# Kernel optimization log

Hardware: AMD Instinct MI355X
Metric: run time of the kernel (lower is better)

The kernel has to match this reference:

```python
import jax, jax.numpy as jnp
import numpy as np

T, B, D, NH, DH, MEM = 1024, 4, 1024, 8, 128, 1024
LIM = 1024  # PositionalEmbedding lim default


def setup_inputs() -> dict:
    key = jax.random.key(0)
    ks = jax.random.split(key, 11)
    h = jax.random.normal(ks[0], (T, B, D), jnp.float32)
    m = jax.random.normal(ks[1], (MEM, B, D), jnp.float32)
    q_w = jax.random.normal(ks[2], (NH * DH, D), jnp.float32) * 0.02
    k_w = jax.random.normal(ks[3], (NH * DH, D), jnp.float32) * 0.02
    r_w = jax.random.normal(ks[4], (NH * DH, D), jnp.float32) * 0.02
    k_bias = jax.random.normal(ks[5], (NH, DH), jnp.float32)  # torch init normal(0,1)
    r_bias = jax.random.normal(ks[6], (NH, DH), jnp.float32)
    ln_scale = jnp.ones((D,), jnp.float32)
    ln_bias = jnp.zeros((D,), jnp.float32)
    reset = jax.random.uniform(ks[7], (T, B)) < 0.01       # sparse episode resets
    old_reset = jax.random.uniform(ks[8], (MEM, B)) < 0.01
    return dict(h=h, m=m, q_w=q_w, k_w=k_w, r_w=r_w, k_bias=k_bias, r_bias=r_bias,
                ln_scale=ln_scale, ln_bias=ln_bias, reset=reset, old_reset=old_reset)


def layer_norm(x, scale, bias, eps=1e-5):
    mu = jnp.mean(x, axis=-1, keepdims=True)
    var = jnp.mean(jnp.square(x - mu), axis=-1, keepdims=True)
    return (x - mu) * jax.lax.rsqrt(var + eps) * scale + bias


def rel_shift(x):
    # x: [T, C, B, N] -> Transformer-XL relative shift
    t, c = x.shape[:2]
    tail = x.shape[2:]
    zero_pad = jnp.zeros((t, 1) + tail, x.dtype)
    x_padded = jnp.concatenate([zero_pad, x], axis=1).reshape((c + 1, t) + tail)
    return x_padded[1:].reshape(x.shape)


def reference(h, m, q_w, k_w, r_w, k_bias, r_bias, ln_scale, ln_bias, reset, old_reset):
    t, b = h.shape[:2]
    mm = m.shape[0]
    tm = t + mm
    # ---- ResetMasker: cols[i,b,j] = any reset at i' with j < i' <= i ----
    resets = jnp.concatenate([old_reset, reset], 0).astype(jnp.int32)  # [L, B]
    cum = jnp.cumsum(resets, axis=0)                                   # [L, B]
    reset_mask = (cum[-t:, None, :] - cum[None, :, :]) > 0             # [T, L, B]
    reset_mask = reset_mask[:, -tm:]                                   # [T, TM, B]
    # ---- default attention mask ----
    i = jnp.arange(t)[:, None]
    j = jnp.arange(tm)[None, :]
    mask_len = mm + t - MEM
    mask_shift_len = (t - mask_len) if mask_len > 0 else t
    future_mask = j >= i + mm          # triu(ones, M + future=0)
    history_mask = j <= i - mask_shift_len
    default_mask = (future_mask | history_mask)[:, :, None]            # [T, TM, 1]
    mask = (reset_mask | default_mask)[:, :, :, None]                  # [T, TM, B, 1]
    # ---- projections ----
    cat = layer_norm(jnp.concatenate([m, h], axis=0), ln_scale, ln_bias)  # [TM, B, D]
    q = (cat[-t:] @ q_w.T).reshape(t, b, NH, DH)
    k = (cat @ k_w.T).reshape(tm, b, NH, DH)
    score = jnp.einsum('ibnd,jbnd->ijbn', q + k_bias, k)               # [T, TM, B, NH]
    # ---- relative position term ----
    pos_seq = jnp.arange(tm - 1, -1, -1, dtype=h.dtype)
    inv_freq = 2.0 * jnp.pi / LIM ** (jnp.arange(0, D, 2, dtype=jnp.float32) / D)
    sinusoid = pos_seq[:, None] * inv_freq                              # [TM, D/2]
    pe = jnp.concatenate([jnp.sin(sinusoid), jnp.cos(sinusoid)], -1)    # [TM, D]
    r = (pe @ r_w.T).reshape(tm, NH, DH)
    pos_score = jnp.einsum('ibnd,jnd->ijbn', q + r_bias, r)             # [T, TM, B, NH]
    score = score + rel_shift(pos_score)
    # ---- scale, mask, clamp, softmax ----
    score = jnp.where(mask, -65000.0, score / np.sqrt(DH))
    score = jnp.clip(score, -65000.0, 65000.0)
    prob = jax.nn.softmax(score, axis=1)
    all_masked = jnp.all(mask, axis=1, keepdims=True)                   # [T, 1, B, 1]
    return jnp.where(all_masked, 0.0, prob)
```

## Files before the change

### kernel.cpp

```cpp
#include <hip/hip_runtime.h>
#include <hip/hip_bf16.h>
#include <stdint.h>

typedef __bf16 bf16;
typedef __bf16 bf16x4 __attribute__((ext_vector_type(4)));
typedef __bf16 bf16x8 __attribute__((ext_vector_type(8)));
typedef float f32x4 __attribute__((ext_vector_type(4)));

__device__ __forceinline__ void gload_lds16(const void* g, void* l) {
  __builtin_amdgcn_global_load_lds((const __attribute__((address_space(1))) void*)g,
                                   (__attribute__((address_space(3))) void*)l, 16, 0, 0);
}

__global__ void setup_kernel(const void* __restrict__ rst, const void* __restrict__ orst,
                             int* __restrict__ jmin) {
  __shared__ int sflag;
  int tid = threadIdx.x;
  if (tid == 0) sflag = 0;
  __syncthreads();
  int local = 0;
  for (int idx = tid; idx < 1024; idx += 256) {
    unsigned v1 = ((const unsigned*)rst)[idx];
    unsigned v2 = ((const unsigned*)orst)[idx];
    unsigned vv[2] = {v1, v2};
    for (int t = 0; t < 2; ++t) {
      unsigned v = vv[t];
      if (v == 0x3F800000u) local |= 1;
      else if (v > 1u) local |= 2;
    }
  }
  if (local) atomicOr(&sflag, local);
  __syncthreads();
  int mode = (sflag & 2) ? 2 : ((sflag & 1) ? 1 : 0);
  int lane = tid & 63, w = tid >> 6;
  if (w < 4) {
    int b = w;
    int rv[32];
    int lmax = -1;
#pragma unroll
    for (int u = 0; u < 32; ++u) {
      int s = lane * 32 + u;
      int idx = (s < 1024) ? s * 4 + b : (s - 1024) * 4 + b;
      const void* p = (s < 1024) ? orst : rst;
      int x;
      if (mode == 2)      x = ((const unsigned char*)p)[idx] != 0;
      else if (mode == 1) x = ((const float*)p)[idx] != 0.0f;
      else                x = ((const int*)p)[idx] != 0;
      rv[u] = x;
      if (x) lmax = s;
    }
    int inc = lmax;
    for (int o = 1; o < 64; o <<= 1) {
      int oth = __shfl_up(inc, o);
      if (lane >= o && oth > inc) inc = oth;
    }
    int cur = __shfl_up(inc, 1);
    if (lane == 0) cur = -1;
#pragma unroll
    for (int u = 0; u < 32; ++u) {
      int s = lane * 32 + u;
      if (rv[u]) cur = s;
      if (s >= 1024) jmin[(s - 1024) * 4 + b] = (cur > 0) ? cur : 0;
    }
  }
}

__global__ __launch_bounds__(256) void ln_kernel(const float* __restrict__ h, const float* __restrict__ mm,
                                                 const float* __restrict__ sc, const float* __restrict__ bi,
                                                 bf16* __restrict__ catln) {
  int row = blockIdx.x;
  const float* src = (row < 4096) ? (mm + (size_t)row * 1024) : (h + (size_t)(row - 4096) * 1024);
  int tid = threadIdx.x;
  float4 v = ((const float4*)src)[tid];
  float s1 = v.x + v.y + v.z + v.w;
  float s2 = v.x * v.x + v.y * v.y + v.z * v.z + v.w * v.w;
  int lane = tid & 63, w = tid >> 6;
  for (int o = 32; o; o >>= 1) { s1 += __shfl_down(s1, o); s2 += __shfl_down(s2, o); }
  __shared__ float red[8];
  if (lane == 0) { red[w] = s1; red[w + 4] = s2; }
  __syncthreads();
  float S1 = red[0] + red[1] + red[2] + red[3];
  float S2 = red[4] + red[5] + red[6] + red[7];
  float mean = S1 * (1.0f / 1024.0f);
  float var = S2 * (1.0f / 1024.0f) - mean * mean;
  float rstd = rsqrtf(var + 1e-5f);
  bf16x4 o;
#pragma unroll
  for (int c = 0; c < 4; ++c) {
    float x = (c == 0) ? v.x : (c == 1) ? v.y : (c == 2) ? v.z : v.w;
    o[c] = (bf16)((x - mean) * rstd * sc[tid * 4 + c] + bi[tid * 4 + c]);
  }
  *(bf16x4*)(catln + (size_t)row * 1024 + tid * 4) = o;
}

__global__ __launch_bounds__(256) void prep_kernel(const float* __restrict__ qw, const float* __restrict__ kw,
                                                   const float* __restrict__ rw, bf16* __restrict__ qwb,
                                                   bf16* __restrict__ kwb, bf16* __restrict__ rwb,
                                                   bf16* __restrict__ pe) {
  size_t id = (size_t)blockIdx.x * 256 + threadIdx.x;
  if (id < 3145728) {
    const float* s = id < 1048576 ? qw : (id < 2097152 ? kw : rw);
    bf16* d = id < 1048576 ? qwb : (id < 2097152 ? kwb : rwb);
    size_t o = id & 1048575;
    d[o] = (bf16)s[o];
  } else {
    size_t p = id - 3145728;
    int jj = (int)(p >> 10), dcol = (int)(p & 1023);
    float pos = (float)(2047 - jj);
    int fi = dcol < 512 ? dcol : dcol - 512;
    float f = exp2f(-0.01953125f * (float)fi);
    float rev = pos * f;
    rev -= floorf(rev);
    float ang = 6.283185307179586f * rev;
    pe[p] = (bf16)(dcol < 512 ? __sinf(ang) : __cosf(ang));
  }
}

__device__ __forceinline__ size_t out_index(int mode, int row, int col) {
  int n = col >> 7, dh = col & 127;
  if (mode <= 0) { int i = row >> 2, b = row & 3; return ((size_t)(b * 8 + n) * 1024 + i) * 128 + dh; }
  if (mode == 1) { int s = row >> 2, b = row & 3; return ((size_t)(b * 8 + n) * 2048 + s) * 128 + dh; }
  return ((size_t)n * 2048 + row) * 128 + dh;
}

__global__ __launch_bounds__(256) void gemm_all(const bf16* __restrict__ catln, const bf16* __restrict__ pe,
                                                const bf16* __restrict__ qwb, const bf16* __restrict__ kwb,
                                                const bf16* __restrict__ rwb, const float* __restrict__ kbias,
                                                const float* __restrict__ rbias, bf16* __restrict__ qkb,
                                                bf16* __restrict__ qrb, bf16* __restrict__ kkv,
                                                bf16* __restrict__ rrv) {
  __shared__ alignas(16) char lA[8192];
  __shared__ alignas(16) char lB[8192];
  const int K = 1024;
  int by = blockIdx.y;
  const bf16* A; const bf16* W; int mode; int brow;
  if (by < 32)      { mode = 0; A = catln + (size_t)4096 * 1024; W = qwb; brow = by << 7; }
  else if (by < 96) { mode = 1; A = catln;                        W = kwb; brow = (by - 32) << 7; }
  else              { mode = 2; A = pe;                           W = rwb; brow = (by - 96) << 7; }
  int tid = threadIdx.x;
  int lane = tid & 63, w = tid >> 6;
  int bcol = blockIdx.x << 7;
  int wr = w >> 1, wc = w & 1;
  f32x4 acc[4][4] = {};
  int r0 = tid >> 2;
  int c8 = (tid & 3) << 3;
  const bf16* gA0 = A + (size_t)(brow + r0) * K + c8;
  const bf16* gB0 = W + (size_t)(bcol + r0) * K + c8;
  char* lAw = lA + w * 1024;
  char* lBw = lB + w * 1024;
  for (int k0 = 0; k0 < K; k0 += 32) {
    if (k0) __syncthreads();
    gload_lds16(gA0 + k0, lAw);
    gload_lds16(gA0 + (size_t)64 * K + k0, lAw + 4096);
    gload_lds16(gB0 + k0, lBw);
    gload_lds16(gB0 + (size_t)64 * K + k0, lBw + 4096);
    __syncthreads();
    const char* pa = lA + (((wr << 6) + (lane & 15)) << 6) + ((lane >> 4) << 4);
    const char* pb = lB + (((wc << 6) + (lane & 15)) << 6) + ((lane >> 4) << 4);
    bf16x8 af[4], bfr[4];
#pragma unroll
    for (int x = 0; x < 4; ++x) {
      af[x] = *(const bf16x8*)(pa + (x << 10));
      bfr[x] = *(const bf16x8*)(pb + (x << 10));
    }
#pragma unroll
    for (int mi = 0; mi < 4; ++mi)
#pragma unroll
      for (int ni = 0; ni < 4; ++ni)
        acc[mi][ni] = __builtin_amdgcn_mfma_f32_16x16x32_bf16(af[mi], bfr[ni], acc[mi][ni], 0, 0, 0);
  }
  int rowb = brow + (wr << 6) + ((lane >> 4) << 2);
  int colb = bcol + (wc << 6) + (lane & 15);
#pragma unroll
  for (int mi = 0; mi < 4; ++mi)
#pragma unroll
    for (int ni = 0; ni < 4; ++ni) {
      int col = colb + (ni << 4);
      float bk = 0.0f, br = 0.0f;
      if (mode == 0) { bk = kbias[col]; br = rbias[col]; }
#pragma unroll
      for (int v = 0; v < 4; ++v) {
        int row = rowb + (mi << 4) + v;
        size_t idx = out_index(mode, row, col);
        if (mode == 0) {
          qkb[idx] = (bf16)(acc[mi][ni][v] + bk);
          qrb[idx] = (bf16)(acc[mi][ni][v] + br);
        } else if (mode == 1) {
          kkv[idx] = (bf16)acc[mi][ni][v];
        } else {
          rrv[idx] = (bf16)acc[mi][ni][v];
        }
      }
    }
}

__global__ __launch_bounds__(256, 2) void score2_kernel(const bf16* __restrict__ qk, const bf16* __restrict__ qr,
                                                        const bf16* __restrict__ kk, const bf16* __restrict__ rr,
                                                        const int* __restrict__ jmin, bf16* __restrict__ P,
                                                        float* __restrict__ scaleBuf) {
  __shared__ float sl[64 * 128];
  __shared__ alignas(16) bf16 stg[2][64 * 128];
  __shared__ int jl_s[64];
  int tid = threadIdx.x, lane = tid & 63;
  int w = (tid >> 6) & 3;
  int bid0 = blockIdx.x;
  int bid = ((bid0 & 7) << 7) | (bid0 >> 3);
  int bn = bid >> 5;
  int it = (bid >> 1) & 15;
  int hh = bid & 1;
  int i0 = it << 6;
  int b = bn >> 3, n = bn & 7;
  int r15 = lane & 15, kc = lane >> 4;
  int il0 = w << 4;
  int g4 = kc << 2;
  const float scale = 0.08838834764831845f;

  if (tid < 64) jl_s[tid] = jmin[(i0 + tid) * 4 + b];

  bf16x8 aK[4], aR[4];
  {
    const bf16* qkrow = qk + ((size_t)bn * 1024 + i0 + il0 + r15) * 128 + kc * 8;
    const bf16* qrrow = qr + ((size_t)bn * 1024 + i0 + il0 + r15) * 128 + kc * 8;
#pragma unroll
    for (int ks = 0; ks < 4; ++ks) {
      aK[ks] = *(const bf16x8*)(qkrow + ks * 32);
      aR[ks] = *(const bf16x8*)(qrrow + ks * 32);
    }
  }

  int su1 = tid, su2 = tid + 256;
  int srow1 = su1 >> 4, scol1 = (su1 & 15) ^ (srow1 & 7);
  int srow2 = su2 >> 4, scol2 = (su2 & 15) ^ (srow2 & 7);
  size_t do1 = (size_t)(su1 & ~63) * 16;
  size_t do2 = (size_t)(su2 & ~63) * 16;
  const bf16* rbase = rr + (size_t)n * 2048 * 128;
  const bf16* kbase = kk + (size_t)bn * 2048 * 128;

  auto issue_pair = [&](int pg) {
    if (pg >= 20) return;
    char* bufb = (char*)stg + (size_t)(pg & 1) * 16384;
#pragma unroll
    for (int k = 0; k < 2; ++k) {
      int ti = pg * 2 + k;
      int ci = ti / 10, si = ti - ci * 10;
      int gc = (hh << 2) + ci;
      const bf16* base = (si < 4) ? rbase : kbase;
      int row0 = (si < 4) ? (1023 + (gc << 7) + (si << 5)) : (i0 + (gc << 7) + ((si - 4) << 5));
      char* db = bufb + (size_t)k * 8192;
      gload_lds16(base + (size_t)(row0 + srow1) * 128 + scol1 * 8, db + do1);
      gload_lds16(base + (size_t)(row0 + srow2) * 128 + scol2 * 8, db + do2);
    }
  };

  int xsw = (((il0 >> 2) + kc) & 7) << 4;
  f32x4 s2r[8];

  issue_pair(0);
  for (int cl = 0; cl < 4; ++cl) {
    int gc = (hh << 2) + cl;
    int c128 = gc << 7;
#pragma unroll
    for (int q = 0; q < 5; ++q) {
      int g = cl * 5 + q;
      __syncthreads();
      issue_pair(g + 1);
      const char* pb = (const char*)stg + (size_t)(g & 1) * 16384;
      __builtin_amdgcn_s_setprio(1);
      if (q < 2) {
#pragma unroll
        for (int sc = 0; sc < 4; ++sc) {
          const char* sb = pb + (sc >> 1) * 8192;
          int fr = ((sc & 1) << 4) + r15;
          f32x4 acc = {};
#pragma unroll
          for (int ks = 0; ks < 4; ++ks) {
            int lcol = (ks << 2) + kc;
            bf16x8 bf = *(const bf16x8*)(sb + fr * 256 + ((lcol ^ (fr & 7)) << 4));
            acc = __builtin_amdgcn_mfma_f32_16x16x32_bf16(aR[ks], bf, acc, 0, 0, 0);
          }
          s2r[q * 4 + sc] = acc;
        }
      } else {
#pragma unroll
        for (int sc = 0; sc < 4; ++sc) {
          int jl0 = ((q - 2) << 6) + (sc << 4);
          int doff = jl0 - il0;
          if (doff < -15 || doff > 142) continue;
          const char* sb = pb + (sc >> 1) * 8192;
          int fr = ((sc & 1) << 4) + r15;
          f32x4 acc = {};
#pragma unroll
          for (int ks = 0; ks < 4; ++ks) {
            int lcol = (ks << 2) + kc;
            bf16x8 bf = *(const bf16x8*)(sb + fr * 256 + ((lcol ^ (fr & 7)) << 4));
            acc = __builtin_amdgcn_mfma_f32_16x16x32_bf16(aK[ks], bf, acc, 0, 0, 0);
          }
          int dbase = jl0 + r15 - il0 - g4;
#pragma unroll
          for (int v = 0; v < 4; ++v) {
            int ddl = dbase - v;
            if ((unsigned)ddl < 128u) {
              sl[(il0 + g4 + v) * 128 + (ddl ^ xsw)] = acc[v];
            }
          }
        }
      }
      __builtin_amdgcn_s_setprio(0);
      if (q == 4) {
#pragma unroll
        for (int v = 0; v < 4; ++v) {
          int il = il0 + g4 + v;
          int ig = i0 + il;
          int jm = jl_s[il];
          int lo = (ig + 1 > jm) ? ig + 1 : jm;
          int ddlo = lo - ig;
          float vals[8];
          float mx = -3.0e38f;
#pragma unroll
          for (int u = 0; u < 8; ++u) {
            int ddc = (u << 4) + r15;
            float x = (s2r[u][v] + sl[il * 128 + (ddc ^ xsw)]) * scale;
            x = fminf(fmaxf(x, -65000.0f), 65000.0f);
            float xm = ((c128 + ddc) >= ddlo) ? x : -3.0e38f;
            vals[u] = xm;
            mx = fmaxf(mx, xm);
          }
          for (int o = 8; o; o >>= 1) mx = fmaxf(mx, __shfl_xor(mx, o));
          float sum = 0.0f;
#pragma unroll
          for (int u = 0; u < 8; ++u) {
            float e = (vals[u] > -1.0e38f) ? __expf(vals[u] - mx) : 0.0f;
            vals[u] = e;
            sum += e;
          }
          for (int o = 8; o; o >>= 1) sum += __shfl_xor(sum, o);
          size_t pbase = ((size_t)bn * 1024 + ig) * 1024;
#pragma unroll
          for (int u = 0; u < 8; ++u) {
            int dd = c128 + (u << 4) + r15;
            P[pbase + (((dd >> 3) ^ (bn & 7)) << 3) + (dd & 7)] = (bf16)vals[u];
          }
          if (r15 == 0) {
            float2 ms = make_float2(mx, sum);
            *(float2*)(scaleBuf + (((size_t)ig * 32 + bn) * 8 + gc) * 2) = ms;
          }
        }
      }
    }
  }
}

__global__ __launch_bounds__(256) void score_full(const bf16* __restrict__ qk, const bf16* __restrict__ qr,
                                                  const bf16* __restrict__ kk, const bf16* __restrict__ rr,
                                                  const int* __restrict__ jmin, float* __restrict__ out) {
  __shared__ float sl[16 * 1024];
  int tid = threadIdx.x, lane = tid & 63, w = tid >> 6;
  int bid = blockIdx.x;
  int i0 = (bid & 63) << 4;
  int bn = bid >> 6;
  int b = bn >> 3, n = bn & 7;
  int r15 = lane & 15, kc = lane >> 4;
  bf16x8 aq[4], ar[4];
  {
    const bf16* qkrow = qk + ((size_t)bn * 1024 + i0 + r15) * 128 + kc * 8;
    const bf16* qrrow = qr + ((size_t)bn * 1024 + i0 + r15) * 128 + kc * 8;
#pragma unroll
    for (int f = 0; f < 4; ++f) {
      aq[f] = *(const bf16x8*)(qkrow + f * 32);
      ar[f] = *(const bf16x8*)(qrrow + f * 32);
    }
  }
  for (int t = w; t < 64; t += 4) {
    int dd0 = t << 4;
    const bf16* rrow = rr + ((size_t)n * 2048 + 1023 + dd0 + r15) * 128 + kc * 8;
    f32x4 acc = {};
#pragma unroll
    for (int f = 0; f < 4; ++f)
      acc = __builtin_amdgcn_mfma_f32_16x16x32_bf16(ar[f], *(const bf16x8*)(rrow + f * 32), acc, 0, 0, 0);
    int dd = dd0 + r15;
#pragma unroll
    for (int v = 0; v < 4; ++v) sl[(kc * 4 + v) * 1024 + dd] = acc[v];
  }
  __syncthreads();
  for (int t = w; t < 65; t += 4) {
    int j0 = i0 + (t << 4);
    const bf16* krow = kk + ((size_t)bn * 2048 + j0 + r15) * 128 + kc * 8;
    f32x4 acc = {};
#pragma unroll
    for (int f = 0; f < 4; ++f)
      acc = __builtin_amdgcn_mfma_f32_16x16x32_bf16(aq[f], *(const bf16x8*)(krow + f * 32), acc, 0, 0, 0);
    int jc = (t << 4) + r15;
#pragma unroll
    for (int v = 0; v < 4; ++v) {
      int ii = kc * 4 + v;
      int dd = jc - ii;
      if (dd >= 1 && dd <= 1023) sl[ii * 1024 + dd] += acc[v];
    }
  }
  __syncthreads();
  const float scale = 0.08838834764831845f;
  for (int ii = w; ii < 16; ii += 4) {
    int i = i0 + ii;
    int jm = jmin[i * 4 + b];
    int lo = (i + 1 > jm) ? i + 1 : jm;
    int ddlo = lo - i;
    size_t ob = (size_t)i * 65536 + bn;
    if (ddlo > 1023) {
      for (int j = lane; j < 2048; j += 64) out[ob + (size_t)j * 32] = 0.0f;
      continue;
    }
    float vals[16];
    float mx = -3.0e38f;
#pragma unroll
    for (int c = 0; c < 16; ++c) {
      int dd = (c << 6) + lane;
      float x = sl[ii * 1024 + dd] * scale;
      x = fminf(fmaxf(x, -65000.0f), 65000.0f);
      float xm = (dd >= ddlo) ? x : -3.0e38f;
      vals[c] = xm;
      mx = fmaxf(mx, xm);
    }
    for (int o = 32; o; o >>= 1) mx = fmaxf(mx, __shfl_xor(mx, o));
    float sum = 0.0f;
#pragma unroll
    for (int c = 0; c < 16; ++c) {
      float e = (vals[c] > -1.0e38f) ? __expf(vals[c] - mx) : 0.0f;
      vals[c] = e;
      sum += e;
    }
    for (int o = 32; o; o >>= 1) sum += __shfl_xor(sum, o);
    float inv = 1.0f / sum;
    for (int j = lane; j < 2048; j += 64) {
      int dd = j - i;
      float pv = 0.0f;
      if (dd >= ddlo && dd <= 1023) {
        float x = sl[ii * 1024 + dd] * scale;
        x = fminf(fmaxf(x, -65000.0f), 65000.0f);
        pv = __expf(x - mx) * inv;
      }
      out[ob + (size_t)j * 32] = pv;
    }
  }
}

__global__ __launch_bounds__(256) void scatter_kernel(const bf16* __restrict__ P,
                                                      const float* __restrict__ scaleBuf,
                                                      float* __restrict__ out) {
  __shared__ alignas(16) bf16 ld[32 * 1024];
  __shared__ float sc_l[32 * 8];
  int i = blockIdx.x;
  int tid = threadIdx.x;
#pragma unroll
  for (int it = 0; it < 16; ++it) {
    int c = it * 256 + tid;
    int bn = c >> 7, u = c & 127;
    const bf16* src = P + ((size_t)bn * 1024 + i) * 1024 + u * 8;
    gload_lds16(src, (char*)ld + (size_t)(it * 256 + (tid & ~63)) * 16);
  }
  {
    int bn_t = tid >> 3, c_t = tid & 7;
    const float2* sp = (const float2*)(scaleBuf + ((size_t)i * 32 + bn_t) * 16);
    float m[8], s[8];
#pragma unroll
    for (int k = 0; k < 8; ++k) { float2 p = sp[k]; m[k] = p.x; s[k] = p.y; }
    float M = m[0];
#pragma unroll
    for (int k = 1; k < 8; ++k) M = fmaxf(M, m[k]);
    float S = 0.0f;
#pragma unroll
    for (int k = 0; k < 8; ++k) S += s[k] * __expf(m[k] - M);
    sc_l[bn_t * 8 + c_t] = (S > 0.0f) ? (__expf(m[c_t] - M) / S) : 0.0f;
  }
  __syncthreads();
  int bn0 = (tid & 7) << 2;
  int jb = tid >> 3;
  size_t ob = (size_t)i * 65536;
  for (int it = 0; it < 64; ++it) {
    int j = it * 32 + jb;
    int dd = j - i;
    f32x4 v = {0.0f, 0.0f, 0.0f, 0.0f};
    if (dd >= 1 && dd <= 1023) {
      int u = dd >> 3, lo = (dd & 7) << 1, cc = dd >> 7;
#pragma unroll
      for (int e = 0; e < 4; ++e) {
        int bn = bn0 + e;
        const bf16* p = (const bf16*)((const char*)ld + bn * 2048 + (((u ^ (bn & 7)) << 4) | lo));
        v[e] = (float)*p * sc_l[bn * 8 + cc];
      }
    }
    *(f32x4*)(out + ob + (size_t)j * 32 + bn0) = v;
  }
}

extern "C" void kernel_launch(void* const* d_in, const int* in_sizes, int n_in,
                              void* d_out, int out_size, void* d_ws, size_t ws_size,
                              hipStream_t stream) {
  const float* h   = (const float*)d_in[0];
  const float* m   = (const float*)d_in[1];
  const float* qw  = (const float*)d_in[2];
  const float* kw  = (const float*)d_in[3];
  const float* rw  = (const float*)d_in[4];
  const float* kb  = (const float*)d_in[5];
  const float* rb  = (const float*)d_in[6];
  const float* lns = (const float*)d_in[7];
  const float* lnb = (const float*)d_in[8];
  const void*  rst = d_in[9];
  const void* orst = d_in[10];
  float* out = (float*)d_out;
  char* ws = (char*)d_ws;

  int* jmin   = (int*)ws;
  bf16* catln = (bf16*)(ws + 65536);
  bf16* qwb   = catln + (size_t)8192 * 1024;
  bf16* kwb   = qwb + (size_t)1024 * 1024;
  bf16* rwb   = kwb + (size_t)1024 * 1024;
  bf16* pe    = rwb + (size_t)1024 * 1024;
  bf16* qkb   = pe + (size_t)2048 * 1024;
  bf16* qrb   = qkb + (size_t)4096 * 1024;
  bf16* kk    = qrb + (size_t)4096 * 1024;
  bf16* rr    = kk + (size_t)8192 * 1024;
  bf16* P     = rr + (size_t)2048 * 1024;
  float* scaleBuf = (float*)(P + (size_t)33554432);
  size_t need_fast = (size_t)((char*)(scaleBuf + 524288) - ws);
  bool fast = ws_size >= need_fast;

  setup_kernel<<<1, 256, 0, stream>>>(rst, orst, jmin);
  ln_kernel<<<8192, 256, 0, stream>>>(h, m, lns, lnb, catln);
  prep_kernel<<<20480, 256, 0, stream>>>(qw, kw, rw, qwb, kwb, rwb, pe);
  gemm_all<<<dim3(8, 112), 256, 0, stream>>>(catln, pe, qwb, kwb, rwb, kb, rb, qkb, qrb, kk, rr);
  if (fast) {
    score2_kernel<<<1024, 256, 0, stream>>>(qkb, qrb, kk, rr, jmin, P, scaleBuf);
    scatter_kernel<<<1024, 256, 0, stream>>>(P, scaleBuf, out);
  } else {
    score_full<<<2048, 256, 0, stream>>>(qkb, qrb, kk, rr, jmin, out);
  }
}
```

Measured before the change: 218.4 us.

## Fuse preprocessing kernels and vectorize scatter with new LDS swizzle

```diff
diff --git a/kernel.cpp b/kernel.cpp
--- a/kernel.cpp
+++ b/kernel.cpp
@@ -12,107 +12,106 @@
                                    (__attribute__((address_space(3))) void*)l, 16, 0, 0);
 }
 
-__global__ void setup_kernel(const void* __restrict__ rst, const void* __restrict__ orst,
-                             int* __restrict__ jmin) {
-  __shared__ int sflag;
+__global__ __launch_bounds__(256) void pre_kernel(const float* __restrict__ h, const float* __restrict__ mm,
+                                                  const float* __restrict__ sc, const float* __restrict__ bi,
+                                                  bf16* __restrict__ catln, const float* __restrict__ qw,
+                                                  const float* __restrict__ kw, const float* __restrict__ rw,
+                                                  bf16* __restrict__ qwb, bf16* __restrict__ kwb,
+                                                  bf16* __restrict__ rwb, bf16* __restrict__ pe,
+                                                  const void* __restrict__ rst, const void* __restrict__ orst,
+                                                  int* __restrict__ jmin) {
+  int bx = blockIdx.x;
   int tid = threadIdx.x;
-  if (tid == 0) sflag = 0;
-  __syncthreads();
-  int local = 0;
-  for (int idx = tid; idx < 1024; idx += 256) {
-    unsigned v1 = ((const unsigned*)rst)[idx];
-    unsigned v2 = ((const unsigned*)orst)[idx];
-    unsigned vv[2] = {v1, v2};
-    for (int t = 0; t < 2; ++t) {
-      unsigned v = vv[t];
-      if (v == 0x3F800000u) local |= 1;
-      else if (v > 1u) local |= 2;
-    }
-  }
-  if (local) atomicOr(&sflag, local);
-  __syncthreads();
-  int mode = (sflag & 2) ? 2 : ((sflag & 1) ? 1 : 0);
-  int lane = tid & 63, w = tid >> 6;
-  if (w < 4) {
-    int b = w;
-    int rv[32];
-    int lmax = -1;
-#pragma unroll
-    for (int u = 0; u < 32; ++u) {
-      int s = lane * 32 + u;
-      int idx = (s < 1024) ? s * 4 + b : (s - 1024) * 4 + b;
-      const void* p = (s < 1024) ? orst : rst;
-      int x;
-      if (mode == 2)      x = ((const unsigned char*)p)[idx] != 0;
-      else if (mode == 1) x = ((const float*)p)[idx] != 0.0f;
-      else                x = ((const int*)p)[idx] != 0;
-      rv[u] = x;
-      if (x) lmax = s;
-    }
-    int inc = lmax;
-    for (int o = 1; o < 64; o <<= 1) {
-      int oth = __shfl_up(inc, o);
-      if (lane >= o && oth > inc) inc = oth;
-    }
-    int cur = __shfl_up(inc, 1);
-    if (lane == 0) cur = -1;
-#pragma unroll
-    for (int u = 0; u < 32; ++u) {
-      int s = lane * 32 + u;
-      if (rv[u]) cur = s;
-      if (s >= 1024) jmin[(s - 1024) * 4 + b] = (cur > 0) ? cur : 0;
-    }
-  }
-}
-
-__global__ __launch_bounds__(256) void ln_kernel(const float* __restrict__ h, const float* __restrict__ mm,
-                                                 const float* __restrict__ sc, const float* __restrict__ bi,
-                                                 bf16* __restrict__ catln) {
-  int row = blockIdx.x;
-  const float* src = (row < 4096) ? (mm + (size_t)row * 1024) : (h + (size_t)(row - 4096) * 1024);
-  int tid = threadIdx.x;
-  float4 v = ((const float4*)src)[tid];
-  float s1 = v.x + v.y + v.z + v.w;
-  float s2 = v.x * v.x + v.y * v.y + v.z * v.z + v.w * v.w;
-  int lane = tid & 63, w = tid >> 6;
-  for (int o = 32; o; o >>= 1) { s1 += __shfl_down(s1, o); s2 += __shfl_down(s2, o); }
-  __shared__ float red[8];
-  if (lane == 0) { red[w] = s1; red[w + 4] = s2; }
-  __syncthreads();
-  float S1 = red[0] + red[1] + red[2] + red[3];
-  float S2 = red[4] + red[5] + red[6] + red[7];
-  float mean = S1 * (1.0f / 1024.0f);
-  float var = S2 * (1.0f / 1024.0f) - mean * mean;
-  float rstd = rsqrtf(var + 1e-5f);
-  bf16x4 o;
-#pragma unroll
-  for (int c = 0; c < 4; ++c) {
-    float x = (c == 0) ? v.x : (c == 1) ? v.y : (c == 2) ? v.z : v.w;
-    o[c] = (bf16)((x - mean) * rstd * sc[tid * 4 + c] + bi[tid * 4 + c]);
-  }
-  *(bf16x4*)(catln + (size_t)row * 1024 + tid * 4) = o;
-}
-
-__global__ __launch_bounds__(256) void prep_kernel(const float* __restrict__ qw, const float* __restrict__ kw,
-                                                   const float* __restrict__ rw, bf16* __restrict__ qwb,
-                                                   bf16* __restrict__ kwb, bf16* __restrict__ rwb,
-                                                   bf16* __restrict__ pe) {
-  size_t id = (size_t)blockIdx.x * 256 + threadIdx.x;
-  if (id < 3145728) {
-    const float* s = id < 1048576 ? qw : (id < 2097152 ? kw : rw);
-    bf16* d = id < 1048576 ? qwb : (id < 2097152 ? kwb : rwb);
-    size_t o = id & 1048575;
-    d[o] = (bf16)s[o];
+  if (bx < 8192) {
+    int row = bx;
+    const float* src = (row < 4096) ? (mm + (size_t)row * 1024) : (h + (size_t)(row - 4096) * 1024);
+    float4 v = ((const float4*)src)[tid];
+    float s1 = v.x + v.y + v.z + v.w;
+    float s2 = v.x * v.x + v.y * v.y + v.z * v.z + v.w * v.w;
+    int lane = tid & 63, w = tid >> 6;
+    for (int o = 32; o; o >>= 1) { s1 += __shfl_down(s1, o); s2 += __shfl_down(s2, o); }
+    __shared__ float red[8];
+    if (lane == 0) { red[w] = s1; red[w + 4] = s2; }
+    __syncthreads();
+    float S1 = red[0] + red[1] + red[2] + red[3];
+    float S2 = red[4] + red[5] + red[6] + red[7];
+    float mean = S1 * (1.0f / 1024.0f);
+    float var = S2 * (1.0f / 1024.0f) - mean * mean;
+    float rstd = rsqrtf(var + 1e-5f);
+    bf16x4 o;
+#pragma unroll
+    for (int c = 0; c < 4; ++c) {
+      float x = (c == 0) ? v.x : (c == 1) ? v.y : (c == 2) ? v.z : v.w;
+      o[c] = (bf16)((x - mean) * rstd * sc[tid * 4 + c] + bi[tid * 4 + c]);
+    }
+    *(bf16x4*)(catln + (size_t)row * 1024 + tid * 4) = o;
+  } else if (bx < 28672) {
+    size_t id = (size_t)(bx - 8192) * 256 + tid;
+    if (id < 3145728) {
+      const float* s = id < 1048576 ? qw : (id < 2097152 ? kw : rw);
+      bf16* d = id < 1048576 ? qwb : (id < 2097152 ? kwb : rwb);
+      size_t o = id & 1048575;
+      d[o] = (bf16)s[o];
+    } else {
+      size_t p = id - 3145728;
+      int jj = (int)(p >> 10), dcol = (int)(p & 1023);
+      float pos = (float)(2047 - jj);
+      int fi = dcol < 512 ? dcol : dcol - 512;
+      float f = exp2f(-0.01953125f * (float)fi);
+      float rev = pos * f;
+      rev -= floorf(rev);
+      float ang = 6.283185307179586f * rev;
+      pe[p] = (bf16)(dcol < 512 ? __sinf(ang) : __cosf(ang));
+    }
   } else {
-    size_t p = id - 3145728;
-    int jj = (int)(p >> 10), dcol = (int)(p & 1023);
-    float pos = (float)(2047 - jj);
-    int fi = dcol < 512 ? dcol : dcol - 512;
-    float f = exp2f(-0.01953125f * (float)fi);
-    float rev = pos * f;
-    rev -= floorf(rev);
-    float ang = 6.283185307179586f * rev;
-    pe[p] = (bf16)(dcol < 512 ? __sinf(ang) : __cosf(ang));
+    __shared__ int sflag;
+    if (tid == 0) sflag = 0;
+    __syncthreads();
+    int local = 0;
+    for (int idx = tid; idx < 1024; idx += 256) {
+      unsigned v1 = ((const unsigned*)rst)[idx];
+      unsigned v2 = ((const unsigned*)orst)[idx];
+      unsigned vv[2] = {v1, v2};
+      for (int t = 0; t < 2; ++t) {
+        unsigned v = vv[t];
+        if (v == 0x3F800000u) local |= 1;
+        else if (v > 1u) local |= 2;
+      }
+    }
+    if (local) atomicOr(&sflag, local);
+    __syncthreads();
+    int mode = (sflag & 2) ? 2 : ((sflag & 1) ? 1 : 0);
+    int lane = tid & 63, w = tid >> 6;
+    if (w < 4) {
+      int b = w;
+      int rv[32];
+      int lmax = -1;
+#pragma unroll
+      for (int u = 0; u < 32; ++u) {
+        int s = lane * 32 + u;
+        int idx = (s < 1024) ? s * 4 + b : (s - 1024) * 4 + b;
+        const void* p = (s < 1024) ? orst : rst;
+        int x;
+        if (mode == 2)      x = ((const unsigned char*)p)[idx] != 0;
+        else if (mode == 1) x = ((const float*)p)[idx] != 0.0f;
+        else                x = ((const int*)p)[idx] != 0;
+        rv[u] = x;
+        if (x) lmax = s;
+      }
+      int inc = lmax;
+      for (int o = 1; o < 64; o <<= 1) {
+        int oth = __shfl_up(inc, o);
+        if (lane >= o && oth > inc) inc = oth;
+      }
+      int cur = __shfl_up(inc, 1);
+      if (lane == 0) cur = -1;
+#pragma unroll
+      for (int u = 0; u < 32; ++u) {
+        int s = lane * 32 + u;
+        if (rv[u]) cur = s;
+        if (s >= 1024) jmin[(s - 1024) * 4 + b] = (cur > 0) ? cur : 0;
+      }
+    }
   }
 }
 
@@ -214,6 +213,7 @@
   int il0 = w << 4;
   int g4 = kc << 2;
   const float scale = 0.08838834764831845f;
+  int psw = (bn >> 1) & 7;
 
   if (tid < 64) jl_s[tid] = jmin[(i0 + tid) * 4 + b];
 
@@ -338,7 +338,7 @@
 #pragma unroll
           for (int u = 0; u < 8; ++u) {
             int dd = c128 + (u << 4) + r15;
-            P[pbase + (((dd >> 3) ^ (bn & 7)) << 3) + (dd & 7)] = (bf16)vals[u];
+            P[pbase + (((dd >> 3) ^ psw) << 3) + (dd & 7)] = (bf16)vals[u];
           }
           if (r15 == 0) {
             float2 ms = make_float2(mx, sum);
@@ -473,22 +473,43 @@
   }
   __syncthreads();
   int bn0 = (tid & 7) << 2;
-  int jb = tid >> 3;
+  int jg = tid >> 3;
   size_t ob = (size_t)i * 65536;
-  for (int it = 0; it < 64; ++it) {
-    int j = it * 32 + jb;
-    int dd = j - i;
-    f32x4 v = {0.0f, 0.0f, 0.0f, 0.0f};
-    if (dd >= 1 && dd <= 1023) {
-      int u = dd >> 3, lo = (dd & 7) << 1, cc = dd >> 7;
-#pragma unroll
-      for (int e = 0; e < 4; ++e) {
-        int bn = bn0 + e;
-        const bf16* p = (const bf16*)((const char*)ld + bn * 2048 + (((u ^ (bn & 7)) << 4) | lo));
-        v[e] = (float)*p * sc_l[bn * 8 + cc];
-      }
-    }
-    *(f32x4*)(out + ob + (size_t)j * 32 + bn0) = v;
+  float scv[4][8];
+#pragma unroll
+  for (int e = 0; e < 4; ++e)
+#pragma unroll
+    for (int cc = 0; cc < 8; ++cc) scv[e][cc] = sc_l[(bn0 + e) * 8 + cc];
+#pragma unroll
+  for (int iter = 0; iter < 8; ++iter) {
+    int dd0 = 4 * jg + 128 * iter;
+    int u = dd0 >> 3, half = (dd0 >> 2) & 1;
+    bf16x4 be[4];
+#pragma unroll
+    for (int e = 0; e < 4; ++e) {
+      int bn = bn0 + e;
+      int swu = u ^ ((bn >> 1) & 7);
+      be[e] = *(const bf16x4*)((const char*)ld + bn * 2048 + (swu << 4) + half * 8);
+    }
+#pragma unroll
+    for (int jj = 0; jj < 4; ++jj) {
+      int j = i + dd0 + jj;
+      f32x4 v;
+#pragma unroll
+      for (int e = 0; e < 4; ++e) v[e] = (float)be[e][jj] * scv[e][iter];
+      *(f32x4*)(out + ob + (size_t)j * 32 + bn0) = v;
+    }
+  }
+  f32x4 z = {0.0f, 0.0f, 0.0f, 0.0f};
+#pragma unroll
+  for (int iter = 0; iter < 8; ++iter) {
+    int z0 = 4 * jg + 128 * iter;
+#pragma unroll
+    for (int jj = 0; jj < 4; ++jj) {
+      int zz = z0 + jj;
+      int j = (zz < i) ? zz : zz + 1024;
+      *(f32x4*)(out + ob + (size_t)j * 32 + bn0) = z;
+    }
   }
 }
 
@@ -524,9 +545,8 @@
   size_t need_fast = (size_t)((char*)(scaleBuf + 524288) - ws);
   bool fast = ws_size >= need_fast;
 
-  setup_kernel<<<1, 256, 0, stream>>>(rst, orst, jmin);
-  ln_kernel<<<8192, 256, 0, stream>>>(h, m, lns, lnb, catln);
-  prep_kernel<<<20480, 256, 0, stream>>>(qw, kw, rw, qwb, kwb, rwb, pe);
+  pre_kernel<<<28673, 256, 0, stream>>>(h, m, lns, lnb, catln, qw, kw, rw, qwb, kwb, rwb,
+                                        pe, rst, orst, jmin);
   gemm_all<<<dim3(8, 112), 256, 0, stream>>>(catln, pe, qwb, kwb, rwb, kb, rb, qkb, qrb, kk, rr);
   if (fast) {
     score2_kernel<<<1024, 256, 0, stream>>>(qkb, qrb, kk, rr, jmin, P, scaleBuf);
```

Result: faster. 212.7 us (-2.6%).
